# Optimization experiments

Hardware: AMD Instinct MI355X
Metric: run time of the kernel (lower is better)

The kernel has to match this reference:

```python
import jax, jax.numpy as jnp
import numpy as np

# --- GridEncoder config (matches torch-ngp defaults) ---
D = 3                 # input_dim
L = 16                # num_levels
C = 2                 # level_dim
H = 16                # base_resolution
PLS = 2.0             # per_level_scale
LOG2_HASHMAP = 19
MAX_PARAMS = 2 ** LOG2_HASHMAP
PRIMES = (1, 2654435761, 805459861)  # fast_hash primes for D=3
ALIGN_CORNERS = False


def _level_meta():
    """Replicates the offsets computation in GridEncoder.__init__ and the
    kernel's per-level resolution / hash-vs-dense decision."""
    metas = []
    off = 0
    for l in range(L):
        res = int(np.ceil(H * PLS ** l))            # kernel: ceil(exp2(l*S)*H - 1) + 1 == H*2^l here
        full = (res if ALIGN_CORNERS else res + 1) ** D
        params = min(MAX_PARAMS, full)
        params = int(np.ceil(params / 8) * 8)       # pad to multiple of 8
        hashed = full > params                      # kernel: stride > hashmap_size after index loop
        metas.append((off, params, res, hashed))
        off += params
    return metas, off

METAS, TOTAL_PARAMS = _level_meta()


def setup_inputs() -> dict:
    key = jax.random.key(0)
    k1, k2 = jax.random.split(key)
    B = 1048576
    inputs = jax.random.uniform(k1, (B, D), dtype=jnp.float32, minval=-1.0, maxval=1.0)
    # reset_parameters(): uniform(-1e-4, 1e-4)
    embeddings = jax.random.uniform(k2, (TOTAL_PARAMS, C), dtype=jnp.float32,
                                    minval=-1e-4, maxval=1e-4)
    return {"inputs": inputs, "embeddings": embeddings}


def _grid_encode(x, embeddings):
    """x: [B, D] in [0, 1]. Returns [B, L*C]."""
    corner_bits = jnp.array([[(c >> d) & 1 for d in range(D)] for c in range(2 ** D)],
                            dtype=jnp.uint32)                       # [8, D]
    primes = jnp.array(PRIMES, dtype=jnp.uint32)
    outs = []
    for l, (off, size, res, hashed) in enumerate(METAS):
        scale = float(np.exp2(l) * H - 1.0)                          # exp2(l*S)*H - 1, S = log2(2) = 1
        pos = x * scale + (0.0 if ALIGN_CORNERS else 0.5)            # [B, D]
        pg_f = jnp.floor(pos)
        frac = pos - pg_f                                            # [B, D] linear interp weights
        pg = pg_f.astype(jnp.uint32)                                 # [B, D]
        corners = pg[None, :, :] + corner_bits[:, None, :]           # [8, B, D]
        # N-linear interpolation weights: prod over dims of frac / (1-frac)
        w = jnp.prod(jnp.where(corner_bits[:, None, :] == 1,
                               frac[None, :, :], 1.0 - frac[None, :, :]), axis=-1)  # [8, B]
        if hashed:
            # fast_hash: xor of pos_grid[d] * primes[d] in wrapping uint32
            idx = corners[..., 0] * primes[0]
            for d in range(1, D):
                idx = idx ^ (corners[..., d] * primes[d])
        else:
            base = res if ALIGN_CORNERS else res + 1
            stride = jnp.array([base ** d for d in range(D)], dtype=jnp.uint32)
            idx = (corners * stride).sum(axis=-1).astype(jnp.uint32)
        idx = (idx % jnp.uint32(size)) + jnp.uint32(off)             # [8, B]
        emb = embeddings[idx]                                        # [8, B, C] gather
        outs.append(jnp.einsum('kb,kbc->bc', w, emb))                # [B, C]
    return jnp.concatenate(outs, axis=-1)                            # [B, L*C], level-major


def reference(inputs, embeddings):
    bound = 1.0
    x = (inputs + bound) / (2.0 * bound)   # map to [0, 1]
    return _grid_encode(x, embeddings)
```

## Files before the change

### kernel.cpp

```cpp
#include <hip/hip_runtime.h>
#include <cstdint>


namespace {

using f32x2 = __attribute__((ext_vector_type(2))) float;
using f32x4 = __attribute__((ext_vector_type(4))) float;

__device__ __forceinline__ void level_setup_g(
    float x, float y, float z, uint32_t l,
    uint32_t g[8], float f[6]) {
  uint32_t res = 16u << l;
  float scale = (float)res - 1.0f;
  float px = x * scale + 0.5f;
  float py = y * scale + 0.5f;
  float pz = z * scale + 0.5f;
  float gx = floorf(px), gy = floorf(py), gz = floorf(pz);
  float rx = px - gx, ry = py - gy, rz = pz - gz;
  uint32_t ix = (uint32_t)gx, iy = (uint32_t)gy, iz = (uint32_t)gz;

  if (l >= 3u) {
    uint32_t off = l * 524288u - 1257368u;
    const uint32_t P2 = 2654435761u, P3 = 805459861u;
    uint32_t hy0 = iy * P2, hy1 = hy0 + P2;
    uint32_t hz0 = iz * P3, hz1 = hz0 + P3;
    uint32_t hb[4] = {hy0 ^ hz0, hy1 ^ hz0, hy0 ^ hz1, hy1 ^ hz1};
    uint32_t ix1 = ix + 1u;
#pragma unroll
    for (int j = 0; j < 4; ++j) {
      g[2 * j]     = ((ix  ^ hb[j]) & 0x7FFFFu) + off;
      g[2 * j + 1] = ((ix1 ^ hb[j]) & 0x7FFFFu) + off;
    }
  } else {
    uint32_t off = (l == 0u) ? 0u : ((l == 1u) ? 4920u : 40864u);
    uint32_t base = res + 1u;
    uint32_t bb = base * base;
    uint32_t dy0 = iy * base, dy1 = dy0 + base;
    uint32_t dz0 = iz * bb,   dz1 = dz0 + bb;
#pragma unroll
    for (int c = 0; c < 8; ++c) {
      g[c] = ix + (uint32_t)(c & 1) +
             ((c & 2) ? dy1 : dy0) + ((c & 4) ? dz1 : dz0) + off;
    }
  }
  f[0] = 1.0f - rx; f[1] = rx;
  f[2] = 1.0f - ry; f[3] = ry;
  f[4] = 1.0f - rz; f[5] = rz;
}

__device__ __forceinline__ f32x2 interp8(const f32x2 e[8], const float f[6]) {
  float o0 = 0.0f, o1 = 0.0f;
#pragma unroll
  for (int c = 0; c < 8; ++c) {
    float w = f[c & 1] * f[2 + ((c >> 1) & 1)] * f[4 + ((c >> 2) & 1)];
    o0 = fmaf(w, e[c].x, o0);
    o1 = fmaf(w, e[c].y, o1);
  }
  f32x2 r; r.x = o0; r.y = o1;
  return r;
}

__global__ __launch_bounds__(256) void prep_xyz_kernel(
    const float* __restrict__ in,
    float* __restrict__ X, float* __restrict__ Y, float* __restrict__ Z,
    uint32_t B) {
  uint32_t t = blockIdx.x * 256u + threadIdx.x;
  uint32_t nquad = B >> 2;
  if (t >= nquad) return;
  const f32x4* in4 = reinterpret_cast<const f32x4*>(in);
  f32x4 q0 = __builtin_nontemporal_load(&in4[t * 3 + 0]);
  f32x4 q1 = __builtin_nontemporal_load(&in4[t * 3 + 1]);
  f32x4 q2 = __builtin_nontemporal_load(&in4[t * 3 + 2]);
  f32x4 xv = {q0.x, q0.w, q1.z, q2.y};
  f32x4 yv = {q0.y, q1.x, q1.w, q2.z};
  f32x4 zv = {q0.z, q1.y, q2.x, q2.w};
  xv = (xv + 1.0f) * 0.5f;
  yv = (yv + 1.0f) * 0.5f;
  zv = (zv + 1.0f) * 0.5f;
  reinterpret_cast<f32x4*>(X)[t] = xv;
  reinterpret_cast<f32x4*>(Y)[t] = yv;
  reinterpret_cast<f32x4*>(Z)[t] = zv;
}

template <bool XYZ>
__global__ __launch_bounds__(256, 6) void gather_lm_kernel(
    const float* __restrict__ in,
    const float* __restrict__ X, const float* __restrict__ Y,
    const float* __restrict__ Z,
    const f32x2* __restrict__ emb,
    f32x2* __restrict__ ws,
    uint32_t B) {
  uint32_t l = blockIdx.y;
  uint32_t p0 = blockIdx.x * 512u + threadIdx.x;
  uint32_t p1 = p0 + 256u;
  bool vA = p0 < B, vB = p1 < B;
  if (!vA) return;
  uint32_t p1c = vB ? p1 : p0;

  float xA, yA, zA, xB, yB, zB;
  if (XYZ) {
    xA = X[p0]; yA = Y[p0]; zA = Z[p0];
    xB = X[p1c]; yB = Y[p1c]; zB = Z[p1c];
  } else {
    xA = (__builtin_nontemporal_load(&in[p0 * 3 + 0]) + 1.0f) * 0.5f;
    yA = (__builtin_nontemporal_load(&in[p0 * 3 + 1]) + 1.0f) * 0.5f;
    zA = (__builtin_nontemporal_load(&in[p0 * 3 + 2]) + 1.0f) * 0.5f;
    xB = (__builtin_nontemporal_load(&in[p1c * 3 + 0]) + 1.0f) * 0.5f;
    yB = (__builtin_nontemporal_load(&in[p1c * 3 + 1]) + 1.0f) * 0.5f;
    zB = (__builtin_nontemporal_load(&in[p1c * 3 + 2]) + 1.0f) * 0.5f;
  }

  uint32_t gA[8]; float fA[6];
  level_setup_g(xA, yA, zA, l, gA, fA);
  f32x2 eA[8];
#pragma unroll
  for (int c = 0; c < 8; ++c) eA[c] = emb[gA[c]];

  uint32_t gB[8]; float fB[6];
  level_setup_g(xB, yB, zB, l, gB, fB);
  f32x2 eB[8];
#pragma unroll
  for (int c = 0; c < 8; ++c) eB[c] = emb[gB[c]];

  f32x2 rA = interp8(eA, fA);
  __builtin_nontemporal_store(rA, &ws[(size_t)l * B + p0]);
  if (vB) {
    f32x2 rB = interp8(eB, fB);
    __builtin_nontemporal_store(rB, &ws[(size_t)l * B + p1]);
  }
}

__global__ __launch_bounds__(256) void transpose_kernel(
    const f32x2* __restrict__ ws,
    f32x4* __restrict__ out,
    uint32_t B) {
  uint32_t n = (B >> 1) * 8u;
  uint32_t t = blockIdx.x * 256u + threadIdx.x;
  if (t >= n) return;
  uint32_t j = t & 7u;
  uint32_t q0 = (t >> 3) * 2u;
  const f32x4* ws4 = reinterpret_cast<const f32x4*>(ws);
  f32x4 va = ws4[((size_t)(2u * j)      * B + q0) >> 1];
  f32x4 vb = ws4[((size_t)(2u * j + 1u) * B + q0) >> 1];
  f32x4 v0 = {va.x, va.y, vb.x, vb.y};
  f32x4 v1 = {va.z, va.w, vb.z, vb.w};
  __builtin_nontemporal_store(v0, &out[(size_t)q0 * 8u + j]);
  __builtin_nontemporal_store(v1, &out[(size_t)(q0 + 1u) * 8u + j]);
}

__global__ __launch_bounds__(256) void grid_encode_fallback(
    const float* __restrict__ in, const f32x2* __restrict__ emb,
    f32x2* __restrict__ out, uint32_t B) {
  uint32_t p = blockIdx.x * 256u + threadIdx.x;
  if (p >= B) return;
  float x = (in[p * 3 + 0] + 1.0f) * 0.5f;
  float y = (in[p * 3 + 1] + 1.0f) * 0.5f;
  float z = (in[p * 3 + 2] + 1.0f) * 0.5f;
#pragma unroll 1
  for (uint32_t l = 0; l < 16u; ++l) {
    uint32_t g[8]; float f[6];
    level_setup_g(x, y, z, l, g, f);
    f32x2 e[8];
#pragma unroll
    for (int c = 0; c < 8; ++c) e[c] = emb[g[c]];
    out[(size_t)p * 16u + l] = interp8(e, f);
  }
}

}

extern "C" void kernel_launch(void* const* d_in, const int* in_sizes, int n_in,
                              void* d_out, int out_size, void* d_ws, size_t ws_size,
                              hipStream_t stream) {
  (void)n_in; (void)out_size;
  const float* in = (const float*)d_in[0];
  const f32x2* emb = (const f32x2*)d_in[1];
  uint32_t B = (uint32_t)(in_sizes[0] / 3);

  size_t ws_lm   = (size_t)16 * B * sizeof(f32x2);
  size_t ws_full = ws_lm + (size_t)3 * B * sizeof(float);

  if ((B % 4u) == 0u && ws_size >= ws_lm) {
    f32x2* ws = (f32x2*)d_ws;
    uint32_t gblocks = (B + 511u) / 512u;
    bool use_xyz = ws_size >= ws_full;
    if (use_xyz) {
      float* X = (float*)((char*)d_ws + ws_lm);
      float* Y = X + B;
      float* Z = Y + B;
      uint32_t pblocks = ((B >> 2) + 255u) / 256u;
      hipLaunchKernelGGL(prep_xyz_kernel, dim3(pblocks), dim3(256), 0, stream,
                         in, X, Y, Z, B);
      hipLaunchKernelGGL((gather_lm_kernel<true>), dim3(gblocks, 16), dim3(256),
                         0, stream, in, X, Y, Z, emb, ws, B);
    } else {
      hipLaunchKernelGGL((gather_lm_kernel<false>), dim3(gblocks, 16), dim3(256),
                         0, stream, in, nullptr, nullptr, nullptr, emb, ws, B);
    }
    uint32_t tblocks = ((B >> 1) * 8u + 255u) / 256u;
    hipLaunchKernelGGL(transpose_kernel, dim3(tblocks), dim3(256), 0, stream,
                       ws, (f32x4*)d_out, B);
  } else {
    uint32_t pblocks = (B + 255u) / 256u;
    hipLaunchKernelGGL(grid_encode_fallback, dim3(pblocks), dim3(256), 0,
                       stream, in, emb, (f32x2*)d_out, B);
  }
}
```

Measured before the change: 599.1 us.

## Gather embedding pairs via aligned 16-byte loads and retune store/transpose paths

The embedding gather now reads the aligned 16-byte pair that contains each corner entry and selects the correct half by index parity. This replaces 8-byte loads with wider aligned loads, at the cost of fetching twice the bytes per corner. Several other changes come with it: results are written to the workspace with an inline-asm sc1 store, the X/Y/Z coordinate loads become nontemporal, the launch-bounds occupancy hint drops from 6 to 5, and the transpose kernel handles two work items per thread. Together these aim to change cache behaviour and raise memory-level parallelism, with risk from the extra gather traffic and lower occupancy.

Result: slower. 765.5 us (+27.8%).

```diff
diff --git a/kernel.cpp b/kernel.cpp
--- a/kernel.cpp
+++ b/kernel.cpp
@@ -7,9 +7,14 @@
 using f32x2 = __attribute__((ext_vector_type(2))) float;
 using f32x4 = __attribute__((ext_vector_type(4))) float;
 
-__device__ __forceinline__ void level_setup_g(
+__device__ __forceinline__ void store_sc1_f32x2(f32x2* p, f32x2 v) {
+  asm volatile("global_store_dwordx2 %0, %1, off sc1"
+               :: "v"(p), "v"(v) : "memory");
+}
+
+__device__ __forceinline__ void corner_pairs(
     float x, float y, float z, uint32_t l,
-    uint32_t g[8], float f[6]) {
+    uint32_t ga[4], uint32_t gb[4], float f[6]) {
   uint32_t res = 16u << l;
   float scale = (float)res - 1.0f;
   float px = x * scale + 0.5f;
@@ -28,8 +33,8 @@
     uint32_t ix1 = ix + 1u;
 #pragma unroll
     for (int j = 0; j < 4; ++j) {
-      g[2 * j]     = ((ix  ^ hb[j]) & 0x7FFFFu) + off;
-      g[2 * j + 1] = ((ix1 ^ hb[j]) & 0x7FFFFu) + off;
+      ga[j] = ((ix  ^ hb[j]) & 0x7FFFFu) + off;
+      gb[j] = ((ix1 ^ hb[j]) & 0x7FFFFu) + off;
     }
   } else {
     uint32_t off = (l == 0u) ? 0u : ((l == 1u) ? 4920u : 40864u);
@@ -37,10 +42,12 @@
     uint32_t bb = base * base;
     uint32_t dy0 = iy * base, dy1 = dy0 + base;
     uint32_t dz0 = iz * bb,   dz1 = dz0 + bb;
-#pragma unroll
-    for (int c = 0; c < 8; ++c) {
-      g[c] = ix + (uint32_t)(c & 1) +
-             ((c & 2) ? dy1 : dy0) + ((c & 4) ? dz1 : dz0) + off;
+    uint32_t dyz[4] = {dy0 + dz0, dy1 + dz0, dy0 + dz1, dy1 + dz1};
+#pragma unroll
+    for (int j = 0; j < 4; ++j) {
+      uint32_t d = ix + dyz[j] + off;
+      ga[j] = d;
+      gb[j] = d + 1u;
     }
   }
   f[0] = 1.0f - rx; f[1] = rx;
@@ -48,13 +55,20 @@
   f[4] = 1.0f - rz; f[5] = rz;
 }
 
-__device__ __forceinline__ f32x2 interp8(const f32x2 e[8], const float f[6]) {
+__device__ __forceinline__ f32x2 consume_pairs(
+    const f32x4 qa[4], const f32x4 qb[4],
+    const uint32_t ga[4], const uint32_t gb[4], const float f[6]) {
   float o0 = 0.0f, o1 = 0.0f;
 #pragma unroll
-  for (int c = 0; c < 8; ++c) {
-    float w = f[c & 1] * f[2 + ((c >> 1) & 1)] * f[4 + ((c >> 2) & 1)];
-    o0 = fmaf(w, e[c].x, o0);
-    o1 = fmaf(w, e[c].y, o1);
+  for (int j = 0; j < 4; ++j) {
+    float wyz = f[2 + (j & 1)] * f[4 + ((j >> 1) & 1)];
+    bool sa = (ga[j] & 1u) != 0u;
+    bool sb = (gb[j] & 1u) != 0u;
+    float eax = sa ? qa[j].z : qa[j].x, eay = sa ? qa[j].w : qa[j].y;
+    float ebx = sb ? qb[j].z : qb[j].x, eby = sb ? qb[j].w : qb[j].y;
+    float wA = f[0] * wyz, wB = f[1] * wyz;
+    o0 = fmaf(wA, eax, fmaf(wB, ebx, o0));
+    o1 = fmaf(wA, eay, fmaf(wB, eby, o1));
   }
   f32x2 r; r.x = o0; r.y = o1;
   return r;
@@ -83,7 +97,7 @@
 }
 
 template <bool XYZ>
-__global__ __launch_bounds__(256, 6) void gather_lm_kernel(
+__global__ __launch_bounds__(256, 5) void gather_lm_kernel(
     const float* __restrict__ in,
     const float* __restrict__ X, const float* __restrict__ Y,
     const float* __restrict__ Z,
@@ -99,8 +113,12 @@
 
   float xA, yA, zA, xB, yB, zB;
   if (XYZ) {
-    xA = X[p0]; yA = Y[p0]; zA = Z[p0];
-    xB = X[p1c]; yB = Y[p1c]; zB = Z[p1c];
+    xA = __builtin_nontemporal_load(&X[p0]);
+    yA = __builtin_nontemporal_load(&Y[p0]);
+    zA = __builtin_nontemporal_load(&Z[p0]);
+    xB = __builtin_nontemporal_load(&X[p1c]);
+    yB = __builtin_nontemporal_load(&Y[p1c]);
+    zB = __builtin_nontemporal_load(&Z[p1c]);
   } else {
     xA = (__builtin_nontemporal_load(&in[p0 * 3 + 0]) + 1.0f) * 0.5f;
     yA = (__builtin_nontemporal_load(&in[p0 * 3 + 1]) + 1.0f) * 0.5f;
@@ -110,23 +128,29 @@
     zB = (__builtin_nontemporal_load(&in[p1c * 3 + 2]) + 1.0f) * 0.5f;
   }
 
-  uint32_t gA[8]; float fA[6];
-  level_setup_g(xA, yA, zA, l, gA, fA);
-  f32x2 eA[8];
-#pragma unroll
-  for (int c = 0; c < 8; ++c) eA[c] = emb[gA[c]];
-
-  uint32_t gB[8]; float fB[6];
-  level_setup_g(xB, yB, zB, l, gB, fB);
-  f32x2 eB[8];
-#pragma unroll
-  for (int c = 0; c < 8; ++c) eB[c] = emb[gB[c]];
-
-  f32x2 rA = interp8(eA, fA);
-  __builtin_nontemporal_store(rA, &ws[(size_t)l * B + p0]);
+  const f32x4* __restrict__ pr = reinterpret_cast<const f32x4*>(emb);
+
+  uint32_t gaA[4], gbA[4]; float fA[6];
+  corner_pairs(xA, yA, zA, l, gaA, gbA, fA);
+  f32x4 qaA[4], qbA[4];
+#pragma unroll
+  for (int j = 0; j < 4; ++j) qaA[j] = pr[gaA[j] >> 1];
+#pragma unroll
+  for (int j = 0; j < 4; ++j) qbA[j] = pr[gbA[j] >> 1];
+
+  uint32_t gaB[4], gbB[4]; float fB[6];
+  corner_pairs(xB, yB, zB, l, gaB, gbB, fB);
+  f32x4 qaB[4], qbB[4];
+#pragma unroll
+  for (int j = 0; j < 4; ++j) qaB[j] = pr[gaB[j] >> 1];
+#pragma unroll
+  for (int j = 0; j < 4; ++j) qbB[j] = pr[gbB[j] >> 1];
+
+  f32x2 rA = consume_pairs(qaA, qbA, gaA, gbA, fA);
+  store_sc1_f32x2(&ws[(size_t)l * B + p0], rA);
   if (vB) {
-    f32x2 rB = interp8(eB, fB);
-    __builtin_nontemporal_store(rB, &ws[(size_t)l * B + p1]);
+    f32x2 rB = consume_pairs(qaB, qbB, gaB, gbB, fB);
+    store_sc1_f32x2(&ws[(size_t)l * B + p1], rB);
   }
 }
 
@@ -134,18 +158,28 @@
     const f32x2* __restrict__ ws,
     f32x4* __restrict__ out,
     uint32_t B) {
-  uint32_t n = (B >> 1) * 8u;
+  uint32_t half = B * 2u;
   uint32_t t = blockIdx.x * 256u + threadIdx.x;
-  if (t >= n) return;
-  uint32_t j = t & 7u;
-  uint32_t q0 = (t >> 3) * 2u;
+  if (t >= half) return;
   const f32x4* ws4 = reinterpret_cast<const f32x4*>(ws);
-  f32x4 va = ws4[((size_t)(2u * j)      * B + q0) >> 1];
-  f32x4 vb = ws4[((size_t)(2u * j + 1u) * B + q0) >> 1];
-  f32x4 v0 = {va.x, va.y, vb.x, vb.y};
-  f32x4 v1 = {va.z, va.w, vb.z, vb.w};
-  __builtin_nontemporal_store(v0, &out[(size_t)q0 * 8u + j]);
-  __builtin_nontemporal_store(v1, &out[(size_t)(q0 + 1u) * 8u + j]);
+
+  uint32_t u0 = t, u1 = t + half;
+  uint32_t j0 = u0 & 7u, q00 = (u0 >> 3) * 2u;
+  uint32_t j1 = u1 & 7u, q10 = (u1 >> 3) * 2u;
+
+  f32x4 va0 = ws4[((size_t)(2u * j0)      * B + q00) >> 1];
+  f32x4 vb0 = ws4[((size_t)(2u * j0 + 1u) * B + q00) >> 1];
+  f32x4 va1 = ws4[((size_t)(2u * j1)      * B + q10) >> 1];
+  f32x4 vb1 = ws4[((size_t)(2u * j1 + 1u) * B + q10) >> 1];
+
+  f32x4 w00 = {va0.x, va0.y, vb0.x, vb0.y};
+  f32x4 w01 = {va0.z, va0.w, vb0.z, vb0.w};
+  f32x4 w10 = {va1.x, va1.y, vb1.x, vb1.y};
+  f32x4 w11 = {va1.z, va1.w, vb1.z, vb1.w};
+  __builtin_nontemporal_store(w00, &out[(size_t)q00 * 8u + j0]);
+  __builtin_nontemporal_store(w01, &out[(size_t)(q00 + 1u) * 8u + j0]);
+  __builtin_nontemporal_store(w10, &out[(size_t)q10 * 8u + j1]);
+  __builtin_nontemporal_store(w11, &out[(size_t)(q10 + 1u) * 8u + j1]);
 }
 
 __global__ __launch_bounds__(256) void grid_encode_fallback(
@@ -156,14 +190,17 @@
   float x = (in[p * 3 + 0] + 1.0f) * 0.5f;
   float y = (in[p * 3 + 1] + 1.0f) * 0.5f;
   float z = (in[p * 3 + 2] + 1.0f) * 0.5f;
+  const f32x4* __restrict__ pr = reinterpret_cast<const f32x4*>(emb);
 #pragma unroll 1
   for (uint32_t l = 0; l < 16u; ++l) {
-    uint32_t g[8]; float f[6];
-    level_setup_g(x, y, z, l, g, f);
-    f32x2 e[8];
-#pragma unroll
-    for (int c = 0; c < 8; ++c) e[c] = emb[g[c]];
-    out[(size_t)p * 16u + l] = interp8(e, f);
+    uint32_t ga[4], gb[4]; float f[6];
+    corner_pairs(x, y, z, l, ga, gb, f);
+    f32x4 qa[4], qb[4];
+#pragma unroll
+    for (int j = 0; j < 4; ++j) qa[j] = pr[ga[j] >> 1];
+#pragma unroll
+    for (int j = 0; j < 4; ++j) qb[j] = pr[gb[j] >> 1];
+    out[(size_t)p * 16u + l] = consume_pairs(qa, qb, ga, gb, f);
   }
 }
 
@@ -197,7 +234,7 @@
       hipLaunchKernelGGL((gather_lm_kernel<false>), dim3(gblocks, 16), dim3(256),
                          0, stream, in, nullptr, nullptr, nullptr, emb, ws, B);
     }
-    uint32_t tblocks = ((B >> 1) * 8u + 255u) / 256u;
+    uint32_t tblocks = (B * 2u + 255u) / 256u;
     hipLaunchKernelGGL(transpose_kernel, dim3(tblocks), dim3(256), 0, stream,
                        ws, (f32x4*)d_out, B);
   } else {
```
